# Optimization experiments

Hardware: AMD Instinct MI355X
Metric: run time of the kernel (lower is better)

## Reference

```python
import jax, jax.numpy as jnp
import numpy as np

B, S, H, NH = 8, 1024, 768, 12
I = 3072
HD = H // NH  # 64


def setup_inputs() -> dict:
    key = jax.random.key(0)
    ks = jax.random.split(key, 6)
    w = lambda k, shape: jax.random.normal(k, shape, jnp.float32) * 0.02
    return {
        "x": jax.random.normal(ks[0], (B, S, H), jnp.float32),
        "ln1_g": jnp.ones((H,), jnp.float32),
        "ln1_b": jnp.zeros((H,), jnp.float32),
        "qkv_w": w(ks[1], (H, 3 * H)),
        "qkv_b": jnp.zeros((3 * H,), jnp.float32),
        "proj_w": w(ks[2], (H, H)),
        "proj_b": jnp.zeros((H,), jnp.float32),
        "ln2_g": jnp.ones((H,), jnp.float32),
        "ln2_b": jnp.zeros((H,), jnp.float32),
        "fc1_w": w(ks[3], (H, I)),
        "fc1_b": jnp.zeros((I,), jnp.float32),
        "fc2_w": w(ks[4], (I, H)),
        "fc2_b": jnp.zeros((H,), jnp.float32),
    }


def _layernorm(x, g, b, eps=1e-5):
    m = x.mean(-1, keepdims=True)
    v = x.var(-1, keepdims=True)  # biased variance, matches torch LayerNorm
    return (x - m) * jax.lax.rsqrt(v + eps) * g + b


def _new_gelu(x):
    c = np.float32(np.sqrt(2.0 / np.pi))
    return 0.5 * x * (1.0 + jnp.tanh(c * (x + 0.044715 * x * x * x)))


def reference(x, ln1_g, ln1_b, qkv_w, qkv_b, proj_w, proj_b,
              ln2_g, ln2_b, fc1_w, fc1_b, fc2_w, fc2_b):
    # --- attention sublayer (pre-LN) ---
    h = _layernorm(x, ln1_g, ln1_b)                     # [B,S,H]
    qkv = h @ qkv_w + qkv_b                             # [B,S,3H]
    q, k, v = jnp.split(qkv, 3, axis=-1)
    q = q.reshape(B, S, NH, HD).transpose(0, 2, 1, 3)   # [B,NH,S,HD]
    k = k.reshape(B, S, NH, HD).transpose(0, 2, 1, 3)
    v = v.reshape(B, S, NH, HD).transpose(0, 2, 1, 3)
    scores = jnp.einsum('bhtd,bhsd->bhts', q, k) / np.float32(np.sqrt(HD))
    probs = jax.nn.softmax(scores, axis=-1)             # [B,NH,S,S]
    attn = jnp.einsum('bhts,bhsd->bhtd', probs, v)      # [B,NH,S,HD]
    attn = attn.transpose(0, 2, 1, 3).reshape(B, S, H)
    attn = attn @ proj_w + proj_b
    x = x + attn
    # --- MLP sublayer (pre-LN) ---
    h2 = _layernorm(x, ln2_g, ln2_b)
    m = _new_gelu(h2 @ fc1_w + fc1_b) @ fc2_w + fc2_b
    return x + m
```

## Files before the change

kernel.cpp:

```cpp
#include <hip/hip_runtime.h>
#include <hip/hip_bf16.h>


typedef __attribute__((ext_vector_type(8))) short bf16x8;
typedef __attribute__((ext_vector_type(4))) float f32x4;
typedef const __attribute__((address_space(3))) char* lds_cp;

#define MFMA16(a, b, c) __builtin_amdgcn_mfma_f32_16x16x32_bf16((a), (b), (c), 0, 0, 0)

#define DSR(dst, addr, off) \
    asm volatile("ds_read_b128 %0, %1 offset:" #off : "=v"(dst) : "v"(addr))
#define WAITV8 asm volatile("s_waitcnt vmcnt(8)" ::: "memory")
#define WAITV0 asm volatile("s_waitcnt vmcnt(0)" ::: "memory")
#define WAITLG3 asm volatile("s_waitcnt lgkmcnt(3)" ::: "memory")
#define WAITLG2 asm volatile("s_waitcnt lgkmcnt(2)" ::: "memory")
#define WAITLG1 asm volatile("s_waitcnt lgkmcnt(1)" ::: "memory")
#define WAITLG asm volatile("s_waitcnt lgkmcnt(0)" ::: "memory")
#define SCHEDB __builtin_amdgcn_sched_barrier(0)
#define CVTPK(d, lo, hi) \
    asm("v_cvt_pk_bf16_f32 %0, %1, %2" : "=v"(d) : "v"(lo), "v"(hi))

__device__ inline short f2bf(float x) {
    __hip_bfloat16 h = __float2bfloat16(x);
    return *reinterpret_cast<short*>(&h);
}

__device__ inline void gload_lds16(const void* g, void* lds) {
    __builtin_amdgcn_global_load_lds(
        (const __attribute__((address_space(1))) unsigned int*)g,
        (__attribute__((address_space(3))) unsigned int*)lds,
        16, 0, 0);
}

__global__ __launch_bounds__(256) void transpose_all(
    const float* __restrict__ qkv_w, const float* __restrict__ proj_w,
    const float* __restrict__ fc1_w, const float* __restrict__ fc2_w,
    short* __restrict__ wt_qkv, short* __restrict__ wt_proj,
    short* __restrict__ wt_fc1, short* __restrict__ wt_fc2) {
    int b = blockIdx.x;
    const float* W;
    short* Wt;
    int K, N, nb;
    if (b < 1728) {
        W = qkv_w; Wt = wt_qkv; K = 768; N = 2304; nb = 72;
    } else if (b < 2304) {
        b -= 1728; W = proj_w; Wt = wt_proj; K = 768; N = 768; nb = 24;
    } else if (b < 4608) {
        b -= 2304; W = fc1_w; Wt = wt_fc1; K = 768; N = 3072; nb = 96;
    } else {
        b -= 4608; W = fc2_w; Wt = wt_fc2; K = 3072; N = 768; nb = 24;
    }
    __shared__ float tile[32][33];
    const int tx = threadIdx.x & 31, ty = threadIdx.x >> 5;
    const int n0 = (b % nb) * 32, k0 = (b / nb) * 32;
#pragma unroll
    for (int i = 0; i < 4; ++i)
        tile[ty + i * 8][tx] = W[(size_t)(k0 + ty + i * 8) * N + n0 + tx];
    __syncthreads();
#pragma unroll
    for (int i = 0; i < 4; ++i)
        Wt[(size_t)(n0 + ty + i * 8) * K + k0 + tx] = f2bf(tile[tx][ty + i * 8]);
}

__global__ __launch_bounds__(192) void ln_k(
    const float* __restrict__ x, const float* __restrict__ g,
    const float* __restrict__ b, short* __restrict__ out) {
    const int row = blockIdx.x;
    const int tid = threadIdx.x;
    const float4 v = *reinterpret_cast<const float4*>(&x[(size_t)row * 768 + tid * 4]);
    float s = v.x + v.y + v.z + v.w;
    float sq = v.x * v.x + v.y * v.y + v.z * v.z + v.w * v.w;
#pragma unroll
    for (int off = 32; off >= 1; off >>= 1) {
        s += __shfl_xor(s, off);
        sq += __shfl_xor(sq, off);
    }
    __shared__ float ss[3], ssq[3];
    const int wid = tid >> 6;
    if ((tid & 63) == 0) { ss[wid] = s; ssq[wid] = sq; }
    __syncthreads();
    s = ss[0] + ss[1] + ss[2];
    sq = ssq[0] + ssq[1] + ssq[2];
    const float mean = s * (1.0f / 768.0f);
    const float var = sq * (1.0f / 768.0f) - mean * mean;
    const float rstd = rsqrtf(var + 1e-5f);
    const float4 gg = *reinterpret_cast<const float4*>(&g[tid * 4]);
    const float4 bb = *reinterpret_cast<const float4*>(&b[tid * 4]);
    const float r0 = (v.x - mean) * rstd * gg.x + bb.x;
    const float r1 = (v.y - mean) * rstd * gg.y + bb.y;
    const float r2 = (v.z - mean) * rstd * gg.z + bb.z;
    const float r3 = (v.w - mean) * rstd * gg.w + bb.w;
    unsigned u0, u1;
    CVTPK(u0, r0, r1);
    CVTPK(u1, r2, r3);
    uint2 uv; uv.x = u0; uv.y = u1;
    *reinterpret_cast<uint2*>(&out[(size_t)row * 768 + tid * 4]) = uv;
}

enum { MODE_BF16 = 0, MODE_QKV = 1, MODE_F32RES = 2, MODE_GELU = 3 };

template <int MODE>
__device__ inline void epi_store4(
    const float* v4, int mrow, int nbase, int N,
    const float* __restrict__ resid, float* __restrict__ outf,
    short* __restrict__ outh, short* __restrict__ Qo,
    short* __restrict__ Ko, short* __restrict__ Vto) {
    if constexpr (MODE == MODE_BF16) {
        unsigned u0, u1;
        CVTPK(u0, v4[0], v4[1]);
        CVTPK(u1, v4[2], v4[3]);
        uint2 uv; uv.x = u0; uv.y = u1;
        *reinterpret_cast<uint2*>(&outh[(size_t)mrow * N + nbase]) = uv;
    } else if constexpr (MODE == MODE_GELU) {
        float gl[4];
#pragma unroll
        for (int r = 0; r < 4; ++r) {
            const float vv = v4[r];
            const float u = 0.7978845608028654f * (vv + 0.044715f * vv * vv * vv);
            gl[r] = vv / (1.0f + __expf(-2.0f * u));
        }
        unsigned u0, u1;
        CVTPK(u0, gl[0], gl[1]);
        CVTPK(u1, gl[2], gl[3]);
        uint2 uv; uv.x = u0; uv.y = u1;
        *reinterpret_cast<uint2*>(&outh[(size_t)mrow * N + nbase]) = uv;
    } else if constexpr (MODE == MODE_F32RES) {
        const float4 rs = *reinterpret_cast<const float4*>(&resid[(size_t)mrow * N + nbase]);
        float4 o4;
        o4.x = v4[0] + rs.x;
        o4.y = v4[1] + rs.y;
        o4.z = v4[2] + rs.z;
        o4.w = v4[3] + rs.w;
        *reinterpret_cast<float4*>(&outf[(size_t)mrow * N + nbase]) = o4;
    } else {
        const int bb = mrow >> 10, s = mrow & 1023;
        if (nbase < 768) {
            const int hh = nbase >> 6, d = nbase & 63;
            unsigned u0, u1;
            CVTPK(u0, v4[0] * 0.125f, v4[1] * 0.125f);
            CVTPK(u1, v4[2] * 0.125f, v4[3] * 0.125f);
            uint2 uv; uv.x = u0; uv.y = u1;
            *reinterpret_cast<uint2*>(
                &Qo[(((size_t)(bb * 12 + hh)) * 1024 + s) * 64 + d]) = uv;
        } else if (nbase < 1536) {
            const int c2 = nbase - 768;
            const int hh = c2 >> 6, d = c2 & 63;
            unsigned u0, u1;
            CVTPK(u0, v4[0], v4[1]);
            CVTPK(u1, v4[2], v4[3]);
            uint2 uv; uv.x = u0; uv.y = u1;
            *reinterpret_cast<uint2*>(
                &Ko[(((size_t)(bb * 12 + hh)) * 1024 + s) * 64 + d]) = uv;
        } else {
            const int c2 = nbase - 1536;
            const int hh = c2 >> 6, d = c2 & 63;
#pragma unroll
            for (int r = 0; r < 4; ++r)
                Vto[(((size_t)(bb * 12 + hh)) * 64 + d + r) * 1024 + s] = f2bf(v4[r]);
        }
    }
}

template <int MODE>
__global__ __launch_bounds__(256) void gemm3p(
    const short* __restrict__ A, const short* __restrict__ Wt,
    const float* __restrict__ bias, const float* __restrict__ resid,
    float* __restrict__ outf, short* __restrict__ outh,
    short* __restrict__ Qo, short* __restrict__ Ko, short* __restrict__ Vto,
    int M, int N, int K) {
    __shared__ __attribute__((aligned(128))) short Al[4][4096];
    __shared__ __attribute__((aligned(128))) short Bl[4][4096];
    const int tid = threadIdx.x;
    const int lane = tid & 63;
    const int w = tid >> 6;
    const int wm = w >> 1, wn = w & 1;
    const int m0 = blockIdx.x * 128, n0 = blockIdx.y * 128;

    f32x4 acc[4][4] = {};

    const int srow = tid >> 2;
    const int scol = (((tid & 3) ^ ((tid >> 3) & 3)) * 8);
    const short* Abase = A + (size_t)(m0 + srow) * K + scol;
    const short* Bbase = Wt + (size_t)(n0 + srow) * K + scol;
    const size_t K64 = (size_t)K * 64;
    short* const AlF = &Al[0][0];
    short* const BlF = &Bl[0][0];

    auto stageT = [&](int boS, int k0s) {
        gload_lds16(Abase + k0s,       AlF + boS + w * 512);
        gload_lds16(Abase + K64 + k0s, AlF + boS + 2048 + w * 512);
        gload_lds16(Bbase + k0s,       BlF + boS + w * 512);
        gload_lds16(Bbase + K64 + k0s, BlF + boS + 2048 + w * 512);
    };

    const int l15 = lane & 15, g = lane >> 4;
    const int lcolswz = (g ^ ((l15 >> 1) & 3)) << 4;
    const int aoff = wm * 4096 + l15 * 64 + lcolswz;
    const int boff = wn * 4096 + l15 * 64 + lcolswz;
    const lds_cp AlB = (lds_cp)AlF;
    const lds_cp BlB = (lds_cp)BlF;

    const int NT = K >> 5;

    stageT(0, 0);
    stageT(4096, 32);
    stageT(8192, 64);

    for (int t = 0; t < NT; ++t) {
        if (t == NT - 1) { WAITV0; } else { WAITV8; }
        SCHEDB;
        __builtin_amdgcn_s_barrier();

        const int bo = (t & 3) * 8192;
        const lds_cp Ab = AlB + (bo + aoff);
        const lds_cp Bb = BlB + (bo + boff);
        bf16x8 av0, av1, av2, av3, bv0, bv1, bv2, bv3;
        DSR(av0, Ab, 0);
        DSR(av1, Ab, 1024);
        DSR(av2, Ab, 2048);
        DSR(av3, Ab, 3072);
        DSR(bv0, Bb, 0);
        DSR(bv1, Bb, 1024);
        DSR(bv2, Bb, 2048);
        DSR(bv3, Bb, 3072);

        if (t + 3 < NT) stageT(((t + 3) & 3) * 4096, (t + 3) << 5);

        __builtin_amdgcn_s_setprio(1);
        WAITLG3;
        SCHEDB;
        acc[0][0] = MFMA16(bv0, av0, acc[0][0]);
        acc[1][0] = MFMA16(bv0, av1, acc[1][0]);
        acc[2][0] = MFMA16(bv0, av2, acc[2][0]);
        acc[3][0] = MFMA16(bv0, av3, acc[3][0]);
        WAITLG2;
        SCHEDB;
        acc[0][1] = MFMA16(bv1, av0, acc[0][1]);
        acc[1][1] = MFMA16(bv1, av1, acc[1][1]);
        acc[2][1] = MFMA16(bv1, av2, acc[2][1]);
        acc[3][1] = MFMA16(bv1, av3, acc[3][1]);
        WAITLG1;
        SCHEDB;
        acc[0][2] = MFMA16(bv2, av0, acc[0][2]);
        acc[1][2] = MFMA16(bv2, av1, acc[1][2]);
        acc[2][2] = MFMA16(bv2, av2, acc[2][2]);
        acc[3][2] = MFMA16(bv2, av3, acc[3][2]);
        WAITLG;
        SCHEDB;
        acc[0][3] = MFMA16(bv3, av0, acc[0][3]);
        acc[1][3] = MFMA16(bv3, av1, acc[1][3]);
        acc[2][3] = MFMA16(bv3, av2, acc[2][3]);
        acc[3][3] = MFMA16(bv3, av3, acc[3][3]);
        __builtin_amdgcn_s_setprio(0);
    }

#pragma unroll
    for (int ni = 0; ni < 4; ++ni) {
        const int nbase = n0 + wn * 64 + ni * 16 + g * 4;
        const float4 b4 = *reinterpret_cast<const float4*>(&bias[nbase]);
#pragma unroll
        for (int mi = 0; mi < 4; ++mi) {
            const int mrow = m0 + wm * 64 + mi * 16 + l15;
            float v4[4] = {acc[mi][ni][0] + b4.x, acc[mi][ni][1] + b4.y,
                           acc[mi][ni][2] + b4.z, acc[mi][ni][3] + b4.w};
            epi_store4<MODE>(v4, mrow, nbase, N, resid, outf, outh, Qo, Ko, Vto);
        }
    }
}

__global__ __launch_bounds__(256) void attn_k(
    const short* __restrict__ Q, const short* __restrict__ Kg,
    const short* __restrict__ Vtg, short* __restrict__ out) {
    __shared__ __attribute__((aligned(128))) short Kl[2][64 * 64];
    __shared__ __attribute__((aligned(128))) short Vl[2][64 * 64];
    __shared__ __attribute__((aligned(128))) short Pl[4][16 * 64];
    const int tid = threadIdx.x, lane = tid & 63, w = tid >> 6;
    const int swz = (blockIdx.x & 7) * 192 + (blockIdx.x >> 3);
    const int qt = swz & 15, bh = swz >> 4;
    const int b = bh / 12, h = bh % 12;
    const int q0 = qt * 64 + w * 16;
    const int l15 = lane & 15, g = lane >> 4;

    bf16x8 aq[2];
    const short* Qb = Q + ((size_t)bh * 1024 + q0) * 64;
#pragma unroll
    for (int kk = 0; kk < 2; ++kk)
        aq[kk] = *(const bf16x8*)&Qb[(size_t)l15 * 64 + kk * 32 + g * 8];

    float m_run = -1e30f, l_run = 0.f;
    f32x4 o[4] = {};

    const short* Kb = Kg + (size_t)bh * 1024 * 64;
    const short* Vb = Vtg + (size_t)bh * 64 * 1024;

    const int srr = tid >> 3;
    const int spp = (tid & 7) * 8;
    const int ssc = spp ^ ((srr & 7) << 3);
    auto stage = [&](int buf, int kv0) {
        gload_lds16(Kb + (size_t)(kv0 + srr) * 64 + ssc,        &Kl[buf][w * 512]);
        gload_lds16(Kb + (size_t)(kv0 + 32 + srr) * 64 + ssc,   &Kl[buf][2048 + w * 512]);
        gload_lds16(Vb + (size_t)srr * 1024 + kv0 + ssc,        &Vl[buf][w * 512]);
        gload_lds16(Vb + (size_t)(srr + 32) * 1024 + kv0 + ssc, &Vl[buf][2048 + w * 512]);
    };

    stage(0, 0);
    __syncthreads();

    int buf = 0;
    for (int t = 0; t < 16; ++t) {
        const lds_cp KB = (lds_cp)&Kl[buf][0];
        const lds_cp VB = (lds_cp)&Vl[buf][0];

        bf16x8 kb[4][2];
#pragma unroll
        for (int nk = 0; nk < 4; ++nk) {
            const int R = nk * 16 + l15;
            const int c0 = (g * 8) ^ ((R & 7) << 3);
            const lds_cp a0 = KB + R * 128 + c0 * 2;
            const lds_cp a1 = KB + R * 128 + (c0 ^ 32) * 2;
            DSR(kb[nk][0], a0, 0);
            DSR(kb[nk][1], a1, 0);
        }

        if (t < 15) stage(buf ^ 1, (t + 1) * 64);

        WAITLG;
        SCHEDB;

        f32x4 sc4[4];
#pragma unroll
        for (int nk = 0; nk < 4; ++nk) {
            f32x4 z = {};
            z = MFMA16(kb[nk][0], aq[0], z);
            z = MFMA16(kb[nk][1], aq[1], z);
            sc4[nk] = z;
        }

        float ml = sc4[0][0];
#pragma unroll
        for (int nk = 0; nk < 4; ++nk)
#pragma unroll
            for (int r = 0; r < 4; ++r) ml = fmaxf(ml, sc4[nk][r]);
        ml = fmaxf(ml, __shfl_xor(ml, 16));
        ml = fmaxf(ml, __shfl_xor(ml, 32));
        const float mn = fmaxf(m_run, ml);
        const float alpha = __expf(m_run - mn);
        m_run = mn;
        float padd[4][4];
        float rsum = 0.f;
#pragma unroll
        for (int nk = 0; nk < 4; ++nk)
#pragma unroll
            for (int r = 0; r < 4; ++r) {
                padd[nk][r] = __expf(sc4[nk][r] - mn);
                rsum += padd[nk][r];
            }
        rsum += __shfl_xor(rsum, 16);
        rsum += __shfl_xor(rsum, 32);
        l_run = l_run * alpha + rsum;
#pragma unroll
        for (int dn = 0; dn < 4; ++dn) o[dn] *= alpha;

#pragma unroll
        for (int nk = 0; nk < 4; ++nk) {
            unsigned u0, u1;
            CVTPK(u0, padd[nk][0], padd[nk][1]);
            CVTPK(u1, padd[nk][2], padd[nk][3]);
            const int cc = (nk * 16 + g * 4) ^ ((l15 & 7) << 3);
            uint2 uv; uv.x = u0; uv.y = u1;
            *reinterpret_cast<uint2*>(&Pl[w][l15 * 64 + cc]) = uv;
        }
        bf16x8 pa[2];
#pragma unroll
        for (int kk = 0; kk < 2; ++kk)
            pa[kk] = *(const bf16x8*)&Pl[w][l15 * 64 + ((kk * 32 + g * 8) ^ ((l15 & 7) << 3))];

        bf16x8 vb[4][2];
#pragma unroll
        for (int dn = 0; dn < 4; ++dn) {
            const int R = dn * 16 + l15;
            const int c0 = (g * 8) ^ ((R & 7) << 3);
            const lds_cp a0 = VB + R * 128 + c0 * 2;
            const lds_cp a1 = VB + R * 128 + (c0 ^ 32) * 2;
            DSR(vb[dn][0], a0, 0);
            DSR(vb[dn][1], a1, 0);
        }
        WAITLG;
        SCHEDB;

#pragma unroll
        for (int dn = 0; dn < 4; ++dn) {
            o[dn] = MFMA16(vb[dn][0], pa[0], o[dn]);
            o[dn] = MFMA16(vb[dn][1], pa[1], o[dn]);
        }

        __syncthreads();
        buf ^= 1;
    }

    const float rl = __builtin_amdgcn_rcpf(l_run);
    short* orow = out + ((size_t)(b * 1024) + q0 + l15) * 768 + h * 64;
#pragma unroll
    for (int dn = 0; dn < 4; ++dn) {
        unsigned u0, u1;
        const float v0 = o[dn][0] * rl, v1 = o[dn][1] * rl;
        const float v2 = o[dn][2] * rl, v3 = o[dn][3] * rl;
        CVTPK(u0, v0, v1);
        CVTPK(u1, v2, v3);
        uint2 uv; uv.x = u0; uv.y = u1;
        *reinterpret_cast<uint2*>(&orow[dn * 16 + g * 4]) = uv;
    }
}

extern "C" void kernel_launch(void* const* d_in, const int* in_sizes, int n_in,
                              void* d_out, int out_size, void* d_ws, size_t ws_size,
                              hipStream_t stream) {
    const float* x      = (const float*)d_in[0];
    const float* ln1_g  = (const float*)d_in[1];
    const float* ln1_b  = (const float*)d_in[2];
    const float* qkv_w  = (const float*)d_in[3];
    const float* qkv_b  = (const float*)d_in[4];
    const float* proj_w = (const float*)d_in[5];
    const float* proj_b = (const float*)d_in[6];
    const float* ln2_g  = (const float*)d_in[7];
    const float* ln2_b  = (const float*)d_in[8];
    const float* fc1_w  = (const float*)d_in[9];
    const float* fc1_b  = (const float*)d_in[10];
    const float* fc2_w  = (const float*)d_in[11];
    const float* fc2_b  = (const float*)d_in[12];
    float* outp = (float*)d_out;

    char* ws = (char*)d_ws;
    size_t off = 0;
    auto alloc = [&](size_t bytes) {
        char* p = ws + off;
        off = (off + bytes + 255) & ~(size_t)255;
        return p;
    };
    short* wt_qkv  = (short*)alloc(2304ull * 768 * 2);
    short* wt_proj = (short*)alloc(768ull * 768 * 2);
    short* wt_fc1  = (short*)alloc(3072ull * 768 * 2);
    short* wt_fc2  = (short*)alloc(768ull * 3072 * 2);
    short* hbuf    = (short*)alloc(8192ull * 768 * 2);
    short* Qb      = (short*)alloc(8192ull * 768 * 2);
    short* Kbuf    = (short*)alloc(8192ull * 768 * 2);
    short* Vtb     = (short*)alloc(8192ull * 768 * 2);
    short* attnb   = (short*)alloc(8192ull * 768 * 2);
    float* x2      = (float*)alloc(8192ull * 768 * 4);
    short* mfc     = Qb;
    (void)ws_size; (void)in_sizes; (void)n_in; (void)out_size;

    transpose_all<<<6912, 256, 0, stream>>>(qkv_w, proj_w, fc1_w, fc2_w,
                                            wt_qkv, wt_proj, wt_fc1, wt_fc2);

    ln_k<<<8192, 192, 0, stream>>>(x, ln1_g, ln1_b, hbuf);
    gemm3p<MODE_QKV><<<dim3(64, 18), 256, 0, stream>>>(
        hbuf, wt_qkv, qkv_b, nullptr, nullptr, nullptr, Qb, Kbuf, Vtb, 8192, 2304, 768);
    attn_k<<<1536, 256, 0, stream>>>(Qb, Kbuf, Vtb, attnb);
    gemm3p<MODE_F32RES><<<dim3(64, 6), 256, 0, stream>>>(
        attnb, wt_proj, proj_b, x, x2, nullptr, nullptr, nullptr, nullptr, 8192, 768, 768);

    ln_k<<<8192, 192, 0, stream>>>(x2, ln2_g, ln2_b, hbuf);
    gemm3p<MODE_GELU><<<dim3(64, 24), 256, 0, stream>>>(
        hbuf, wt_fc1, fc1_b, nullptr, nullptr, mfc, nullptr, nullptr, nullptr, 8192, 3072, 768);
    gemm3p<MODE_F32RES><<<dim3(64, 6), 256, 0, stream>>>(
        mfc, wt_fc2, fc2_b, x2, outp, nullptr, nullptr, nullptr, nullptr, 8192, 768, 3072);
}
```

Baseline: 271.9 us.

## Add 256x256-tile 8-wave GEMM kernel for QKV and FC1 projections

Introduces gemm8p, a 512-thread GEMM with 256x256 output tiles, 128KB of dynamic LDS double buffering, and split-phase LDS reads interleaved with async global-to-LDS staging. It replaces the 128x128 gemm3p for the QKV and FC1 projections. Larger tiles raise arithmetic intensity and cut global traffic per FLOP. The cost is fewer blocks (288 and 384 on a 256-CU part), which risks tail imbalance, along with higher register pressure and only one block per CU given the LDS footprint.

```diff
diff --git a/kernel.cpp b/kernel.cpp
--- a/kernel.cpp
+++ b/kernel.cpp
@@ -10,6 +10,7 @@
 
 #define DSR(dst, addr, off) \
     asm volatile("ds_read_b128 %0, %1 offset:" #off : "=v"(dst) : "v"(addr))
+#define WAITV4 asm volatile("s_waitcnt vmcnt(4)" ::: "memory")
 #define WAITV8 asm volatile("s_waitcnt vmcnt(8)" ::: "memory")
 #define WAITV0 asm volatile("s_waitcnt vmcnt(0)" ::: "memory")
 #define WAITLG3 asm volatile("s_waitcnt lgkmcnt(3)" ::: "memory")
@@ -162,6 +163,147 @@
 }
 
 template <int MODE>
+__global__ __launch_bounds__(512, 2) void gemm8p(
+    const short* __restrict__ A, const short* __restrict__ Wt,
+    const float* __restrict__ bias, const float* __restrict__ resid,
+    float* __restrict__ outf, short* __restrict__ outh,
+    short* __restrict__ Qo, short* __restrict__ Ko, short* __restrict__ Vto,
+    int M, int N, int K) {
+    extern __shared__ __attribute__((aligned(128))) char smem[];
+    const int tid = threadIdx.x;
+    const int lane = tid & 63;
+    const int w = tid >> 6;
+    const int wm = w >> 2, wn = w & 3;
+    const int m0 = blockIdx.x * 256, n0 = blockIdx.y * 256;
+    const int l15 = lane & 15, g = lane >> 4;
+
+    f32x4 acc[8][4] = {};
+
+    const int srowb = tid >> 2;
+    const int sul = (((tid & 3) ^ ((tid >> 3) & 3)) * 8);
+    char* const SM = smem;
+    auto stageA = [&](int bs, int ks, int kt) {
+        const short* src = A + (size_t)(m0 + srowb) * K + kt * 64 + ks * 32 + sul;
+        char* dst = SM + bs * 32768 + ks * 16384 + w * 1024;
+        gload_lds16(src, dst);
+        gload_lds16(src + (size_t)128 * K, dst + 8192);
+    };
+    auto stageB = [&](int bs, int ks, int kt) {
+        const short* src = Wt + (size_t)(n0 + srowb) * K + kt * 64 + ks * 32 + sul;
+        char* dst = SM + 65536 + bs * 32768 + ks * 16384 + w * 1024;
+        gload_lds16(src, dst);
+        gload_lds16(src + (size_t)128 * K, dst + 8192);
+    };
+
+    const int swz16 = (g ^ ((l15 >> 1) & 3)) << 4;
+    const int abase = (wm * 128 + l15) * 64 + swz16;
+    const int bbase = 65536 + (wn * 64 + l15) * 64 + swz16;
+    const lds_cp SM3 = (lds_cp)SM;
+
+    const int NT = K >> 6;
+
+    stageA(0, 0, 0);
+    stageB(0, 0, 0);
+    stageA(0, 1, 0);
+    stageB(0, 1, 0);
+
+    for (int t = 0; t < NT; ++t) {
+        const int b = t & 1;
+        const int bs = (t + 1) & 1;
+        int ts = t + 1; if (ts > NT - 1) ts = NT - 1;
+        const int bo = b * 32768;
+        bf16x8 a0, a1, a2, a3, a4, a5, a6, a7, b0, b1, b2, b3;
+
+#define MFMA_NI(NI, BF)                                          \
+        acc[0][NI] = MFMA16(BF, a0, acc[0][NI]);                 \
+        acc[1][NI] = MFMA16(BF, a1, acc[1][NI]);                 \
+        acc[2][NI] = MFMA16(BF, a2, acc[2][NI]);                 \
+        acc[3][NI] = MFMA16(BF, a3, acc[3][NI]);                 \
+        acc[4][NI] = MFMA16(BF, a4, acc[4][NI]);                 \
+        acc[5][NI] = MFMA16(BF, a5, acc[5][NI]);                 \
+        acc[6][NI] = MFMA16(BF, a6, acc[6][NI]);                 \
+        acc[7][NI] = MFMA16(BF, a7, acc[7][NI]);
+
+        WAITV4;
+        SCHEDB;
+        __builtin_amdgcn_s_barrier();
+        {
+            const lds_cp Ap = SM3 + (bo + abase);
+            const lds_cp Bp = SM3 + (bo + bbase);
+            DSR(a0, Ap, 0); DSR(a1, Ap, 1024); DSR(a2, Ap, 2048); DSR(a3, Ap, 3072);
+            DSR(a4, Ap, 4096); DSR(a5, Ap, 5120); DSR(a6, Ap, 6144); DSR(a7, Ap, 7168);
+            DSR(b0, Bp, 0); DSR(b1, Bp, 1024);
+        }
+        stageA(bs, 0, ts);
+        WAITLG;
+        SCHEDB;
+        __builtin_amdgcn_s_setprio(1);
+        MFMA_NI(0, b0)
+        MFMA_NI(1, b1)
+        __builtin_amdgcn_s_setprio(0);
+
+        __builtin_amdgcn_s_barrier();
+        {
+            const lds_cp Bp = SM3 + (bo + bbase);
+            DSR(b2, Bp, 2048); DSR(b3, Bp, 3072);
+        }
+        stageB(bs, 0, ts);
+        WAITLG;
+        SCHEDB;
+        __builtin_amdgcn_s_setprio(1);
+        MFMA_NI(2, b2)
+        MFMA_NI(3, b3)
+        __builtin_amdgcn_s_setprio(0);
+
+        WAITV4;
+        SCHEDB;
+        __builtin_amdgcn_s_barrier();
+        {
+            const lds_cp Ap = SM3 + (bo + 16384 + abase);
+            const lds_cp Bp = SM3 + (bo + 16384 + bbase);
+            DSR(a0, Ap, 0); DSR(a1, Ap, 1024); DSR(a2, Ap, 2048); DSR(a3, Ap, 3072);
+            DSR(a4, Ap, 4096); DSR(a5, Ap, 5120); DSR(a6, Ap, 6144); DSR(a7, Ap, 7168);
+            DSR(b0, Bp, 0); DSR(b1, Bp, 1024);
+        }
+        stageA(bs, 1, ts);
+        WAITLG;
+        SCHEDB;
+        __builtin_amdgcn_s_setprio(1);
+        MFMA_NI(0, b0)
+        MFMA_NI(1, b1)
+        __builtin_amdgcn_s_setprio(0);
+
+        __builtin_amdgcn_s_barrier();
+        {
+            const lds_cp Bp = SM3 + (bo + 16384 + bbase);
+            DSR(b2, Bp, 2048); DSR(b3, Bp, 3072);
+        }
+        stageB(bs, 1, ts);
+        WAITLG;
+        SCHEDB;
+        __builtin_amdgcn_s_setprio(1);
+        MFMA_NI(2, b2)
+        MFMA_NI(3, b3)
+        __builtin_amdgcn_s_setprio(0);
+#undef MFMA_NI
+    }
+    WAITV0;
+
+#pragma unroll
+    for (int ni = 0; ni < 4; ++ni) {
+        const int nbase = n0 + wn * 64 + ni * 16 + g * 4;
+        const float4 b4 = *reinterpret_cast<const float4*>(&bias[nbase]);
+#pragma unroll
+        for (int mi = 0; mi < 8; ++mi) {
+            const int mrow = m0 + wm * 128 + mi * 16 + l15;
+            float v4[4] = {acc[mi][ni][0] + b4.x, acc[mi][ni][1] + b4.y,
+                           acc[mi][ni][2] + b4.z, acc[mi][ni][3] + b4.w};
+            epi_store4<MODE>(v4, mrow, nbase, N, resid, outf, outh, Qo, Ko, Vto);
+        }
+    }
+}
+
+template <int MODE>
 __global__ __launch_bounds__(256) void gemm3p(
     const short* __restrict__ A, const short* __restrict__ Wt,
     const float* __restrict__ bias, const float* __restrict__ resid,
@@ -450,18 +592,27 @@
     short* mfc     = Qb;
     (void)ws_size; (void)in_sizes; (void)n_in; (void)out_size;
 
+    static bool attr_set = false;
+    if (!attr_set) {
+        hipFuncSetAttribute(reinterpret_cast<const void*>(gemm8p<MODE_QKV>),
+                            hipFuncAttributeMaxDynamicSharedMemorySize, 131072);
+        hipFuncSetAttribute(reinterpret_cast<const void*>(gemm8p<MODE_GELU>),
+                            hipFuncAttributeMaxDynamicSharedMemorySize, 131072);
+        attr_set = true;
+    }
+
     transpose_all<<<6912, 256, 0, stream>>>(qkv_w, proj_w, fc1_w, fc2_w,
                                             wt_qkv, wt_proj, wt_fc1, wt_fc2);
 
     ln_k<<<8192, 192, 0, stream>>>(x, ln1_g, ln1_b, hbuf);
-    gemm3p<MODE_QKV><<<dim3(64, 18), 256, 0, stream>>>(
+    gemm8p<MODE_QKV><<<dim3(32, 9), 512, 131072, stream>>>(
         hbuf, wt_qkv, qkv_b, nullptr, nullptr, nullptr, Qb, Kbuf, Vtb, 8192, 2304, 768);
     attn_k<<<1536, 256, 0, stream>>>(Qb, Kbuf, Vtb, attnb);
     gemm3p<MODE_F32RES><<<dim3(64, 6), 256, 0, stream>>>(
         attnb, wt_proj, proj_b, x, x2, nullptr, nullptr, nullptr, nullptr, 8192, 768, 768);
 
     ln_k<<<8192, 192, 0, stream>>>(x2, ln2_g, ln2_b, hbuf);
-    gemm3p<MODE_GELU><<<dim3(64, 24), 256, 0, stream>>>(
+    gemm8p<MODE_GELU><<<dim3(32, 12), 512, 131072, stream>>>(
         hbuf, wt_fc1, fc1_b, nullptr, nullptr, mfc, nullptr, nullptr, nullptr, 8192, 3072, 768);
     gemm3p<MODE_F32RES><<<dim3(64, 6), 256, 0, stream>>>(
         mfc, wt_fc2, fc2_b, x2, outp, nullptr, nullptr, nullptr, nullptr, 8192, 768, 3072);
```

Measured after the change: 288.7 us. 6.2% more time.

## Give each wave private LDS staging to remove block barriers in GEMM

Applied to the files above, without the earlier changes.

The GEMM kernel is restructured so each of the four waves stages its own 64-row A and B slices into a private LDS region, double-buffered, which removes the per-iteration workgroup s_barrier. The next stage is issued after the last LDS read completes, within the MFMA sequence. In exchange, each A and B tile is loaded by two waves (duplicated global/L2 traffic), prefetch depth drops from three stages to two, and LDS use stays at 64KB.

```diff
diff --git a/kernel.cpp b/kernel.cpp
--- a/kernel.cpp
+++ b/kernel.cpp
@@ -162,14 +162,13 @@
 }
 
 template <int MODE>
-__global__ __launch_bounds__(256) void gemm3p(
+__global__ __launch_bounds__(256) void gemm_nb(
     const short* __restrict__ A, const short* __restrict__ Wt,
     const float* __restrict__ bias, const float* __restrict__ resid,
     float* __restrict__ outf, short* __restrict__ outh,
     short* __restrict__ Qo, short* __restrict__ Ko, short* __restrict__ Vto,
     int M, int N, int K) {
-    __shared__ __attribute__((aligned(128))) short Al[4][4096];
-    __shared__ __attribute__((aligned(128))) short Bl[4][4096];
+    __shared__ __attribute__((aligned(128))) short L[32768];
     const int tid = threadIdx.x;
     const int lane = tid & 63;
     const int w = tid >> 6;
@@ -178,42 +177,47 @@
 
     f32x4 acc[4][4] = {};
 
-    const int srow = tid >> 2;
-    const int scol = (((tid & 3) ^ ((tid >> 3) & 3)) * 8);
-    const short* Abase = A + (size_t)(m0 + srow) * K + scol;
-    const short* Bbase = Wt + (size_t)(n0 + srow) * K + scol;
-    const size_t K64 = (size_t)K * 64;
-    short* const AlF = &Al[0][0];
-    short* const BlF = &Bl[0][0];
-
-    auto stageT = [&](int boS, int k0s) {
-        gload_lds16(Abase + k0s,       AlF + boS + w * 512);
-        gload_lds16(Abase + K64 + k0s, AlF + boS + 2048 + w * 512);
-        gload_lds16(Bbase + k0s,       BlF + boS + w * 512);
-        gload_lds16(Bbase + K64 + k0s, BlF + boS + 2048 + w * 512);
+    const int sr = lane >> 2;
+    const int su = (((lane & 3) ^ ((lane >> 3) & 3)) * 8);
+    const short* sA0 = A + (size_t)(m0 + wm * 64 + sr) * K + su;
+    const short* sB0 = Wt + (size_t)(n0 + wn * 64 + sr) * K + su;
+    short* const LF = &L[0];
+    short* const dW = LF + w * 8192;
+
+    auto stage = [&](int p, int kt) {
+        const int k0s = kt << 5;
+        short* dA = dW + p * 4096;
+        short* dB = dA + 2048;
+        const short* a = sA0 + k0s;
+        const short* b = sB0 + k0s;
+        gload_lds16(a,                     dA);
+        gload_lds16(a + (size_t)16 * K,    dA + 512);
+        gload_lds16(a + (size_t)32 * K,    dA + 1024);
+        gload_lds16(a + (size_t)48 * K,    dA + 1536);
+        gload_lds16(b,                     dB);
+        gload_lds16(b + (size_t)16 * K,    dB + 512);
+        gload_lds16(b + (size_t)32 * K,    dB + 1024);
+        gload_lds16(b + (size_t)48 * K,    dB + 1536);
     };
 
     const int l15 = lane & 15, g = lane >> 4;
     const int lcolswz = (g ^ ((l15 >> 1) & 3)) << 4;
-    const int aoff = wm * 4096 + l15 * 64 + lcolswz;
-    const int boff = wn * 4096 + l15 * 64 + lcolswz;
-    const lds_cp AlB = (lds_cp)AlF;
-    const lds_cp BlB = (lds_cp)BlF;
+    const int aoff = w * 16384 + l15 * 64 + lcolswz;
+    const int boff = aoff + 4096;
+    const lds_cp LB = (lds_cp)LF;
 
     const int NT = K >> 5;
 
-    stageT(0, 0);
-    stageT(4096, 32);
-    stageT(8192, 64);
+    stage(0, 0);
+    stage(1, 1);
 
     for (int t = 0; t < NT; ++t) {
-        if (t == NT - 1) { WAITV0; } else { WAITV8; }
-        SCHEDB;
-        __builtin_amdgcn_s_barrier();
-
-        const int bo = (t & 3) * 8192;
-        const lds_cp Ab = AlB + (bo + aoff);
-        const lds_cp Bb = BlB + (bo + boff);
+        if (t < NT - 1) { WAITV8; } else { WAITV0; }
+        SCHEDB;
+
+        const int pb = (t & 1) * 8192;
+        const lds_cp Ab = LB + (aoff + pb);
+        const lds_cp Bb = LB + (boff + pb);
         bf16x8 av0, av1, av2, av3, bv0, bv1, bv2, bv3;
         DSR(av0, Ab, 0);
         DSR(av1, Ab, 1024);
@@ -224,8 +228,6 @@
         DSR(bv2, Bb, 2048);
         DSR(bv3, Bb, 3072);
 
-        if (t + 3 < NT) stageT(((t + 3) & 3) * 4096, (t + 3) << 5);
-
         __builtin_amdgcn_s_setprio(1);
         WAITLG3;
         SCHEDB;
@@ -247,6 +249,7 @@
         acc[3][2] = MFMA16(bv2, av3, acc[3][2]);
         WAITLG;
         SCHEDB;
+        if (t + 2 < NT) stage(t & 1, t + 2);
         acc[0][3] = MFMA16(bv3, av0, acc[0][3]);
         acc[1][3] = MFMA16(bv3, av1, acc[1][3]);
         acc[2][3] = MFMA16(bv3, av2, acc[2][3]);
@@ -454,15 +457,15 @@
                                             wt_qkv, wt_proj, wt_fc1, wt_fc2);
 
     ln_k<<<8192, 192, 0, stream>>>(x, ln1_g, ln1_b, hbuf);
-    gemm3p<MODE_QKV><<<dim3(64, 18), 256, 0, stream>>>(
+    gemm_nb<MODE_QKV><<<dim3(64, 18), 256, 0, stream>>>(
         hbuf, wt_qkv, qkv_b, nullptr, nullptr, nullptr, Qb, Kbuf, Vtb, 8192, 2304, 768);
     attn_k<<<1536, 256, 0, stream>>>(Qb, Kbuf, Vtb, attnb);
-    gemm3p<MODE_F32RES><<<dim3(64, 6), 256, 0, stream>>>(
+    gemm_nb<MODE_F32RES><<<dim3(64, 6), 256, 0, stream>>>(
         attnb, wt_proj, proj_b, x, x2, nullptr, nullptr, nullptr, nullptr, 8192, 768, 768);
 
     ln_k<<<8192, 192, 0, stream>>>(x2, ln2_g, ln2_b, hbuf);
-    gemm3p<MODE_GELU><<<dim3(64, 24), 256, 0, stream>>>(
+    gemm_nb<MODE_GELU><<<dim3(64, 24), 256, 0, stream>>>(
         hbuf, wt_fc1, fc1_b, nullptr, nullptr, mfc, nullptr, nullptr, nullptr, 8192, 3072, 768);
-    gemm3p<MODE_F32RES><<<dim3(64, 6), 256, 0, stream>>>(
+    gemm_nb<MODE_F32RES><<<dim3(64, 6), 256, 0, stream>>>(
         mfc, wt_fc2, fc2_b, x2, outp, nullptr, nullptr, nullptr, nullptr, 8192, 768, 3072);
 }
```

Result: slower. 322.5 us (+18.6%).
